# Optimization experiments

Hardware: AMD Instinct MI355X
Metric: run time of the kernel (lower is better)

Reference implementation:

```python
import jax, jax.numpy as jnp
import numpy as np
import math

# dims: batch, in-channels, freq bins, frames(=cropsize), ffn dim, bands
B, C, BINS, W, FF, NB = 16, 8, 1024, 256, 2048, 4
EPS = 1e-5


def _ln(x, g, b):
    m = x.mean(-1, keepdims=True)
    v = ((x - m) ** 2).mean(-1, keepdims=True)
    return (x - m) / jnp.sqrt(v + EPS) * g + b


def _conv1d(x, w, groups=1):
    # x: [b, Cin, L], w: [Cout, Cin//groups, K], 'same' padding
    pad = (w.shape[-1] - 1) // 2
    return jax.lax.conv_general_dilated(
        x, w, (1,), [(pad, pad)],
        dimension_numbers=('NCH', 'OIH', 'NCH'), feature_group_count=groups)


def _mb_attn(x, mem, qw, qb, kw, kb, vw, vb, ow, ob, er, dist_w):
    # MultibandFrameAttention with skewed relative-position bias
    b, w, c = x.shape
    d = c // NB
    q = (x @ qw.T + qb).reshape(b, w, NB, d).transpose(0, 2, 1, 3)    # [b,nb,w,d]
    k = (mem @ kw.T + kb).reshape(b, w, NB, d).transpose(0, 2, 3, 1)  # [b,nb,d,w]
    v = (mem @ vw.T + vb).reshape(b, w, NB, d).transpose(0, 2, 1, 3)  # [b,nb,w,d]
    # skew trick: q @ er -> pad left on last dim -> transpose -> drop first row
    qer = jnp.einsum('bnwd,dc->bnwc', q, er)                           # [b,nb,w,W]
    skew = jnp.pad(qer, ((0, 0), (0, 0), (0, 0), (1, 0)))
    skew = skew.transpose(0, 1, 3, 2)[:, :, 1:, :]                     # [b,nb,W,w]
    idx = jnp.arange(w)
    dist = jnp.abs(idx[:, None] - idx[None, :]).astype(x.dtype) / 2.0  # [w,w]
    p = dist[None] * dist_w + skew                                     # [b,nb,w,w]
    qk = jnp.einsum('bnwd,bndk->bnwk', q, k) / math.sqrt(c)
    a = jax.nn.softmax(qk + p, axis=-1)
    o = jnp.einsum('bnwk,bnkd->bnwd', a, v).transpose(0, 2, 1, 3).reshape(b, w, c)
    return o @ ow.T + ob


def setup_inputs() -> dict:
    key = jax.random.key(0)
    ks = jax.random.split(key, 24)
    rn = lambda k, s, sc=0.02: jax.random.normal(k, s, dtype=jnp.float32) * sc
    d = BINS // NB
    ones = lambda n: jnp.ones((n,), jnp.float32)
    zeros = lambda n: jnp.zeros((n,), jnp.float32)
    return {
        'x': jax.random.normal(ks[0], (B, C, BINS, W), jnp.float32),
        'bott_w': rn(ks[1], (1, C), 0.3),
        'bn_g': ones(1), 'bn_b': zeros(1), 'bn_m': zeros(1), 'bn_v': ones(1),
        'glu_w': rn(ks[2], (2 * BINS, BINS)),
        'n1g': ones(BINS), 'n1b': zeros(BINS),
        'c1L_w': rn(ks[3], (2 * FF, BINS)),
        'c1R_w': rn(ks[4], (FF // 2, BINS, 3)),
        'n2g': ones(2 * FF), 'n2b': zeros(2 * FF),
        'c2dw_w': rn(ks[5], (2 * FF, 1, 9), 0.1),
        'c2pw_w': rn(ks[6], (FF // 2, 2 * FF)),
        'n3g': ones(BINS), 'n3b': zeros(BINS),
        'qw': rn(ks[7], (BINS, BINS)), 'qb': zeros(BINS),
        'kw': rn(ks[8], (BINS, BINS)), 'kb': zeros(BINS),
        'vw': rn(ks[9], (BINS, BINS)), 'vb': zeros(BINS),
        'ow': rn(ks[10], (BINS, BINS)), 'ob': zeros(BINS),
        'er': rn(ks[11], (d, W), 0.02),
        'dist_w': rn(ks[12], (NB, W, 1), 0.02),
        'n4g': ones(BINS), 'n4b': zeros(BINS),
        'c3_w': rn(ks[13], (2 * FF, BINS)),
        'c4_w': rn(ks[14], (BINS, 2 * FF)),
        'n5g': ones(BINS), 'n5b': zeros(BINS),
    }


def reference(x, bott_w, bn_g, bn_b, bn_m, bn_v, glu_w, n1g, n1b,
              c1L_w, c1R_w, n2g, n2b, c2dw_w, c2pw_w, n3g, n3b,
              qw, qb, kw, kb, vw, vb, ow, ob, er, dist_w,
              n4g, n4b, c3_w, c4_w, n5g, n5b):
    # bottleneck: Linear(C->1) over channel dim, BatchNorm2d(1) eval, ReLU
    h0 = jnp.einsum('bchw,oc->bohw', x, bott_w)                        # [b,1,bins,w]
    h0 = (h0 - bn_m[None, :, None, None]) / jnp.sqrt(bn_v[None, :, None, None] + EPS)
    h0 = jax.nn.relu(h0 * bn_g[None, :, None, None] + bn_b[None, :, None, None])
    xs = h0[:, 0].transpose(0, 2, 1)                                   # [b,w,bins]

    # GLU block
    g = xs @ glu_w.T
    a, bgate = g[..., :BINS], g[..., BINS:]
    xs = _ln(xs + a * jax.nn.sigmoid(bgate), n1g, n1b)

    # conv/linear FFN
    hL = jax.nn.relu(xs @ c1L_w.T)                                     # [b,w,2ff]
    hR = jax.nn.relu(_conv1d(xs.transpose(0, 2, 1), c1R_w).transpose(0, 2, 1))
    hR = jnp.pad(hR, ((0, 0), (0, 0), (0, hL.shape[2] - hR.shape[2])))
    h = _ln(hL + hR, n2g, n2b)
    t = _conv1d(h.transpose(0, 2, 1), c2dw_w, groups=2 * FF)           # depthwise
    t = jnp.einsum('bcl,oc->bol', t, c2pw_w).transpose(0, 2, 1)        # [b,w,ff//2]
    t = jnp.pad(t, ((0, 0), (0, 0), (0, xs.shape[2] - t.shape[2])))
    xs = _ln(xs + t, n3g, n3b)

    # multiband attention (self)
    h = _mb_attn(xs, xs, qw, qb, kw, kb, vw, vb, ow, ob, er, dist_w)
    xs = _ln(xs + h, n4g, n4b)

    # final FFN
    h = jax.nn.relu(xs @ c3_w.T) @ c4_w.T
    xs = _ln(xs + h, n5g, n5b)
    return xs.transpose(0, 2, 1)[:, None]                              # [b,1,bins,w]
```

## Files before the change

### kernel.cpp

```cpp
#include <hip/hip_runtime.h>
#include <hip/hip_bf16.h>

#define EPSF 1e-5f

typedef unsigned short u16;
typedef unsigned int   u32;
typedef __attribute__((ext_vector_type(8))) short bf16x8;
typedef __attribute__((ext_vector_type(4))) float f32x4;

__device__ __forceinline__ u16 f2bf(float f) {
    u32 u = __builtin_bit_cast(u32, f);
    u32 r = u + 0x7fffu + ((u >> 16) & 1u);
    return (u16)(r >> 16);
}
__device__ __forceinline__ float bf2f(u16 h) {
    return __builtin_bit_cast(float, (u32)h << 16);
}
__device__ __forceinline__ float4 bf4f(ushort4 v) {
    return make_float4(bf2f(v.x), bf2f(v.y), bf2f(v.z), bf2f(v.w));
}
__device__ __forceinline__ ushort4 f4bf(float a, float b, float c, float d) {
    ushort4 o; o.x = f2bf(a); o.y = f2bf(b); o.z = f2bf(c); o.w = f2bf(d); return o;
}
__device__ __forceinline__ void gld16(void* lds, const void* gsrc) {
    __builtin_amdgcn_global_load_lds(
        (const __attribute__((address_space(1))) u32*)gsrc,
        (__attribute__((address_space(3))) u32*)lds, 16, 0, 0);
}

__device__ __forceinline__ float wred_sum(float v) {
#pragma unroll
    for (int off = 32; off; off >>= 1) v += __shfl_xor(v, off, 64);
    return v;
}
__device__ __forceinline__ void block_red2(float& s1, float& s2, int tid) {
    __shared__ float red[8];
    s1 = wred_sum(s1); s2 = wred_sum(s2);
    const int lane = tid & 63, wid = tid >> 6;
    if (!lane) { red[wid] = s1; red[4 + wid] = s2; }
    __syncthreads();
    s1 = red[0] + red[1] + red[2] + red[3];
    s2 = red[4] + red[5] + red[6] + red[7];
}

struct SetupArgs {
    const float* ws[9]; u16* wd[9]; int wn[9];
    const float* c1r; u16* c1rd;
    const float* er;  u16* erd;
    const float* dw;  float* dwd;
    const float* qb;  const float* kb; const float* vb; float* bcat;
    u16* zp;
    int off[15];
};
__global__ __launch_bounds__(256)
void setup_k(SetupArgs a)
{
    const int b = blockIdx.x;
    int seg = 0;
    while (seg < 13 && b >= a.off[seg + 1]) ++seg;
    const int i = (b - a.off[seg]) * 256 + threadIdx.x;
    if (seg < 9) {
        if (i < a.wn[seg]) {
            const float4 v = ((const float4*)a.ws[seg])[i];
            ((ushort4*)a.wd[seg])[i] = f4bf(v.x, v.y, v.z, v.w);
        }
    } else if (seg == 9) {
        if (i < 3145728) {
            const int q = i / 3072, rem = i - q * 3072;
            const int ks = rem >> 10, ci = rem & 1023;
            a.c1rd[i] = f2bf(a.c1r[((long)q * 1024 + ci) * 3 + ks]);
        }
    } else if (seg == 10) {
        if (i < 65536) { const int c = i >> 8, d = i & 255; a.erd[i] = f2bf(a.er[d * 256 + c]); }
    } else if (seg == 11) {
        if (i < 36864) { const int k = i >> 12, c = i & 4095; a.dwd[i] = a.dw[c * 9 + k]; }
    } else if (seg == 12) {
        if (i < 3072) { const float* s = (i < 1024) ? a.qb : ((i < 2048) ? a.kb : a.vb); a.bcat[i] = s[i & 1023]; }
    } else {
        if (i < 8192) a.zp[i] = 0;
    }
}

__global__ __launch_bounds__(256)
void bottleneck_k(const float* __restrict__ x, const float* __restrict__ bw,
                  const float* __restrict__ bn_g, const float* __restrict__ bn_b,
                  const float* __restrict__ bn_m, const float* __restrict__ bn_v,
                  u16* __restrict__ xsb)
{
    __shared__ float tile[32][33];
    const int b = blockIdx.z, h0 = blockIdx.y * 32, w0 = blockIdx.x * 32;
    const int tid = threadIdx.x, c = tid & 31, r = tid >> 5;
    float wreg[8];
#pragma unroll
    for (int ch = 0; ch < 8; ++ch) wreg[ch] = bw[ch];
    const float sc = bn_g[0] * rsqrtf(bn_v[0] + EPSF);
    const float sh = bn_b[0] - bn_m[0] * sc;
#pragma unroll
    for (int it = 0; it < 4; ++it) {
        const int h = h0 + r + it * 8;
        const int w = w0 + c;
        float acc = 0.f;
#pragma unroll
        for (int ch = 0; ch < 8; ++ch)
            acc += x[(((long)b * 8 + ch) * 1024 + h) * 256 + w] * wreg[ch];
        tile[r + it * 8][c] = fmaxf(acc * sc + sh, 0.f);
    }
    __syncthreads();
#pragma unroll
    for (int it = 0; it < 4; ++it) {
        const int wl = r + it * 8;
        xsb[((long)b * 256 + w0 + wl) * 1024 + h0 + c] = f2bf(tile[c][wl]);
    }
}

template<int ACT, int OUTBF, int BIAS, int SPLITK>
__global__ __launch_bounds__(512, 2)
void gemm8_k(const u16* __restrict__ A, const u16* __restrict__ B,
             const float* __restrict__ bias, void* __restrict__ Cout,
             int N, int K , int lda, int ldb, long partStride)
{
    extern __shared__ u16 lds[];
    const int m0 = blockIdx.y * 256, n0 = blockIdx.x * 256;
    const int koff = (SPLITK > 1) ? blockIdx.z * K : 0;
    const int nt = K >> 6;
    const int tid = threadIdx.x;
    const int lane = tid & 63, wid = tid >> 6;
    const int wr = ((wid >> 2) & 1) * 128;
    const int wc = (wid & 3) * 64;
    const int l15 = lane & 15, l4 = lane >> 4;

    const u16* Ag = A + (long)m0 * lda + koff;
    const u16* Bg = B + (long)n0 * ldb + koff;

    auto stage = [&](const u16* g, int ld, int ldsbase, int kcol, int h) {
#pragma unroll
        for (int is = 0; is < 2; ++is) {
            const int r = h * 128 + is * 64 + (tid >> 3);
            const int sc = ((tid & 7) * 8) ^ (((r >> 2) & 1) << 4);
            gld16(&lds[ldsbase + h * 8192 + is * 4096 + tid * 8],
                  g + (long)r * ld + kcol + sc);
        }
    };
    auto frag = [&](int base, int row, int col) -> bf16x8 {
        return *(const bf16x8*)&lds[base + row * 64 + (col ^ (((row >> 2) & 1) << 4))];
    };

    f32x4 acc[8][4] = {};

    stage(Ag, lda, 0, 0, 0);
    stage(Ag, lda, 0, 0, 1);
    stage(Bg, ldb, 32768, 0, 0);
    stage(Bg, ldb, 32768, 0, 1);
    if (nt > 1) {
        stage(Bg, ldb, 49152, 64, 0);
        stage(Bg, ldb, 49152, 64, 1);
        stage(Ag, lda, 16384, 64, 0);
        asm volatile("s_waitcnt vmcnt(6)" ::: "memory");
    } else {
        asm volatile("s_waitcnt vmcnt(0)" ::: "memory");
    }
    __builtin_amdgcn_s_barrier();

    for (int kt = 0; kt < nt; ++kt) {
        const int cs = kt & 1;
        const int ab = cs * 16384;
        const int bb = 32768 + cs * 16384;
        const int abn = (cs ^ 1) * 16384;
        const int kc1 = (kt + 1) * 64, kc2 = (kt + 2) * 64;
        bf16x8 alo[4][2], ahi[4][2], b01[2][2], b23[2][2];

#pragma unroll
        for (int i = 0; i < 4; ++i)
#pragma unroll
            for (int kk = 0; kk < 2; ++kk)
                alo[i][kk] = frag(ab, wr + i * 16 + l15, kk * 32 + l4 * 8);
#pragma unroll
        for (int j = 0; j < 2; ++j)
#pragma unroll
            for (int kk = 0; kk < 2; ++kk)
                b01[j][kk] = frag(bb, wc + j * 16 + l15, kk * 32 + l4 * 8);
        if (kt + 1 < nt) stage(Ag, lda, abn, kc1, 1);
        __builtin_amdgcn_s_barrier();
        asm volatile("s_waitcnt lgkmcnt(0)" ::: "memory");
        __builtin_amdgcn_s_setprio(1);
#pragma unroll
        for (int i = 0; i < 4; ++i)
#pragma unroll
            for (int j = 0; j < 2; ++j)
#pragma unroll
                for (int kk = 0; kk < 2; ++kk)
                    acc[i][j] = __builtin_amdgcn_mfma_f32_16x16x32_bf16(alo[i][kk], b01[j][kk], acc[i][j], 0, 0, 0);
        __builtin_amdgcn_s_setprio(0);
        __builtin_amdgcn_s_barrier();

#pragma unroll
        for (int j = 0; j < 2; ++j)
#pragma unroll
            for (int kk = 0; kk < 2; ++kk)
                b23[j][kk] = frag(bb, wc + (j + 2) * 16 + l15, kk * 32 + l4 * 8);
        if (kt + 2 < nt) stage(Bg, ldb, bb, kc2, 0);
        __builtin_amdgcn_s_barrier();
        asm volatile("s_waitcnt lgkmcnt(0)" ::: "memory");
        __builtin_amdgcn_s_setprio(1);
#pragma unroll
        for (int i = 0; i < 4; ++i)
#pragma unroll
            for (int j = 0; j < 2; ++j)
#pragma unroll
                for (int kk = 0; kk < 2; ++kk)
                    acc[i][j + 2] = __builtin_amdgcn_mfma_f32_16x16x32_bf16(alo[i][kk], b23[j][kk], acc[i][j + 2], 0, 0, 0);
        __builtin_amdgcn_s_setprio(0);
        __builtin_amdgcn_s_barrier();

#pragma unroll
        for (int i = 0; i < 4; ++i)
#pragma unroll
            for (int kk = 0; kk < 2; ++kk)
                ahi[i][kk] = frag(ab, wr + (i + 4) * 16 + l15, kk * 32 + l4 * 8);
        if (kt + 2 < nt) stage(Bg, ldb, bb, kc2, 1);
        __builtin_amdgcn_s_barrier();
        asm volatile("s_waitcnt lgkmcnt(0)" ::: "memory");
        __builtin_amdgcn_s_setprio(1);
#pragma unroll
        for (int i = 0; i < 4; ++i)
#pragma unroll
            for (int j = 0; j < 2; ++j)
#pragma unroll
                for (int kk = 0; kk < 2; ++kk)
                    acc[i + 4][j + 2] = __builtin_amdgcn_mfma_f32_16x16x32_bf16(ahi[i][kk], b23[j][kk], acc[i + 4][j + 2], 0, 0, 0);
        __builtin_amdgcn_s_setprio(0);
        __builtin_amdgcn_s_barrier();

        if (kt + 2 < nt) stage(Ag, lda, ab, kc2, 0);
        __builtin_amdgcn_s_barrier();
        __builtin_amdgcn_s_setprio(1);
#pragma unroll
        for (int i = 0; i < 4; ++i)
#pragma unroll
            for (int j = 0; j < 2; ++j)
#pragma unroll
                for (int kk = 0; kk < 2; ++kk)
                    acc[i + 4][j] = __builtin_amdgcn_mfma_f32_16x16x32_bf16(ahi[i][kk], b01[j][kk], acc[i + 4][j], 0, 0, 0);
        __builtin_amdgcn_s_setprio(0);
        if (kt + 2 < nt) {
            asm volatile("s_waitcnt vmcnt(6)" ::: "memory");
        } else {
            asm volatile("s_waitcnt vmcnt(0)" ::: "memory");
        }
        __builtin_amdgcn_s_barrier();
    }

    if (SPLITK > 1) {
        u16* Cp = (u16*)Cout + (long)blockIdx.z * partStride;
#pragma unroll
        for (int i = 0; i < 8; ++i)
#pragma unroll
            for (int j = 0; j < 4; ++j) {
                const int n = n0 + wc + j * 16 + l15;
#pragma unroll
                for (int q = 0; q < 4; ++q) {
                    const int m = m0 + wr + i * 16 + l4 * 4 + q;
                    Cp[(long)m * N + n] = f2bf(acc[i][j][q]);
                }
            }
    } else {
        float* Cf = (float*)Cout;
        u16*   Cb = (u16*)Cout;
#pragma unroll
        for (int i = 0; i < 8; ++i)
#pragma unroll
            for (int j = 0; j < 4; ++j) {
                const int n = n0 + wc + j * 16 + l15;
                const float bv = BIAS ? bias[n] : 0.f;
#pragma unroll
                for (int q = 0; q < 4; ++q) {
                    const int m = m0 + wr + i * 16 + l4 * 4 + q;
                    float v = acc[i][j][q] + bv;
                    if (ACT) v = fmaxf(v, 0.f);
                    if (OUTBF) Cb[(long)m * N + n] = f2bf(v);
                    else       Cf[(long)m * N + n] = v;
                }
            }
    }
}

__global__ __launch_bounds__(512, 2)
void conv38_k(const u16* __restrict__ Xb, const u16* __restrict__ Wt,
              const u16* __restrict__ zp, u16* __restrict__ C)
{
    extern __shared__ u16 lds[];
    const int ks = blockIdx.z;
    const int m0 = blockIdx.y * 256, n0 = blockIdx.x * 256;
    const int nt = 16;
    const int tid = threadIdx.x;
    const int lane = tid & 63, wid = tid >> 6;
    const int wr = ((wid >> 2) & 1) * 128;
    const int wc = (wid & 3) * 64;
    const int l15 = lane & 15, l4 = lane >> 4;

    auto stageA = [&](int ldsbase, int kcol, int h) {
#pragma unroll
        for (int is = 0; is < 2; ++is) {
            const int r = h * 128 + is * 64 + (tid >> 3);
            const int sc = ((tid & 7) * 8) ^ (((r >> 2) & 1) << 4);
            const int t = m0 + r;
            const int wp = (t & 255) + ks - 1;
            const u16* src = ((unsigned)wp < 256u)
                ? Xb + (long)(t + ks - 1) * 1024 + kcol + sc
                : zp;
            gld16(&lds[ldsbase + h * 8192 + is * 4096 + tid * 8], src);
        }
    };
    auto stageB = [&](int ldsbase, int kcol, int h) {
#pragma unroll
        for (int is = 0; is < 2; ++is) {
            const int r = h * 128 + is * 64 + (tid >> 3);
            const int sc = ((tid & 7) * 8) ^ (((r >> 2) & 1) << 4);
            gld16(&lds[ldsbase + h * 8192 + is * 4096 + tid * 8],
                  Wt + (long)(n0 + r) * 3072 + ks * 1024 + kcol + sc);
        }
    };
    auto frag = [&](int base, int row, int col) -> bf16x8 {
        return *(const bf16x8*)&lds[base + row * 64 + (col ^ (((row >> 2) & 1) << 4))];
    };

    f32x4 acc[8][4] = {};

    stageA(0, 0, 0);
    stageA(0, 0, 1);
    stageB(32768, 0, 0);
    stageB(32768, 0, 1);
    stageB(49152, 64, 0);
    stageB(49152, 64, 1);
    stageA(16384, 64, 0);
    asm volatile("s_waitcnt vmcnt(6)" ::: "memory");
    __builtin_amdgcn_s_barrier();

    for (int kt = 0; kt < nt; ++kt) {
        const int cs = kt & 1;
        const int ab = cs * 16384;
        const int bb = 32768 + cs * 16384;
        const int abn = (cs ^ 1) * 16384;
        const int kc1 = (kt + 1) * 64, kc2 = (kt + 2) * 64;
        bf16x8 alo[4][2], ahi[4][2], b01[2][2], b23[2][2];

#pragma unroll
        for (int i = 0; i < 4; ++i)
#pragma unroll
            for (int kk = 0; kk < 2; ++kk)
                alo[i][kk] = frag(ab, wr + i * 16 + l15, kk * 32 + l4 * 8);
#pragma unroll
        for (int j = 0; j < 2; ++j)
#pragma unroll
            for (int kk = 0; kk < 2; ++kk)
                b01[j][kk] = frag(bb, wc + j * 16 + l15, kk * 32 + l4 * 8);
        if (kt + 1 < nt) stageA(abn, kc1, 1);
        __builtin_amdgcn_s_barrier();
        asm volatile("s_waitcnt lgkmcnt(0)" ::: "memory");
        __builtin_amdgcn_s_setprio(1);
#pragma unroll
        for (int i = 0; i < 4; ++i)
#pragma unroll
            for (int j = 0; j < 2; ++j)
#pragma unroll
                for (int kk = 0; kk < 2; ++kk)
                    acc[i][j] = __builtin_amdgcn_mfma_f32_16x16x32_bf16(alo[i][kk], b01[j][kk], acc[i][j], 0, 0, 0);
        __builtin_amdgcn_s_setprio(0);
        __builtin_amdgcn_s_barrier();

#pragma unroll
        for (int j = 0; j < 2; ++j)
#pragma unroll
            for (int kk = 0; kk < 2; ++kk)
                b23[j][kk] = frag(bb, wc + (j + 2) * 16 + l15, kk * 32 + l4 * 8);
        if (kt + 2 < nt) stageB(bb, kc2, 0);
        __builtin_amdgcn_s_barrier();
        asm volatile("s_waitcnt lgkmcnt(0)" ::: "memory");
        __builtin_amdgcn_s_setprio(1);
#pragma unroll
        for (int i = 0; i < 4; ++i)
#pragma unroll
            for (int j = 0; j < 2; ++j)
#pragma unroll
                for (int kk = 0; kk < 2; ++kk)
                    acc[i][j + 2] = __builtin_amdgcn_mfma_f32_16x16x32_bf16(alo[i][kk], b23[j][kk], acc[i][j + 2], 0, 0, 0);
        __builtin_amdgcn_s_setprio(0);
        __builtin_amdgcn_s_barrier();

#pragma unroll
        for (int i = 0; i < 4; ++i)
#pragma unroll
            for (int kk = 0; kk < 2; ++kk)
                ahi[i][kk] = frag(ab, wr + (i + 4) * 16 + l15, kk * 32 + l4 * 8);
        if (kt + 2 < nt) stageB(bb, kc2, 1);
        __builtin_amdgcn_s_barrier();
        asm volatile("s_waitcnt lgkmcnt(0)" ::: "memory");
        __builtin_amdgcn_s_setprio(1);
#pragma unroll
        for (int i = 0; i < 4; ++i)
#pragma unroll
            for (int j = 0; j < 2; ++j)
#pragma unroll
                for (int kk = 0; kk < 2; ++kk)
                    acc[i + 4][j + 2] = __builtin_amdgcn_mfma_f32_16x16x32_bf16(ahi[i][kk], b23[j][kk], acc[i + 4][j + 2], 0, 0, 0);
        __builtin_amdgcn_s_setprio(0);
        __builtin_amdgcn_s_barrier();

        if (kt + 2 < nt) stageA(ab, kc2, 0);
        __builtin_amdgcn_s_barrier();
        __builtin_amdgcn_s_setprio(1);
#pragma unroll
        for (int i = 0; i < 4; ++i)
#pragma unroll
            for (int j = 0; j < 2; ++j)
#pragma unroll
                for (int kk = 0; kk < 2; ++kk)
                    acc[i + 4][j] = __builtin_amdgcn_mfma_f32_16x16x32_bf16(ahi[i][kk], b01[j][kk], acc[i + 4][j], 0, 0, 0);
        __builtin_amdgcn_s_setprio(0);
        if (kt + 2 < nt) {
            asm volatile("s_waitcnt vmcnt(6)" ::: "memory");
        } else {
            asm volatile("s_waitcnt vmcnt(0)" ::: "memory");
        }
        __builtin_amdgcn_s_barrier();
    }

    u16* Cp = C + (long)ks * 4194304;
#pragma unroll
    for (int i = 0; i < 8; ++i)
#pragma unroll
        for (int j = 0; j < 4; ++j) {
            const int n = n0 + wc + j * 16 + l15;
#pragma unroll
            for (int q = 0; q < 4; ++q) {
                const int m = m0 + wr + i * 16 + l4 * 4 + q;
                Cp[(long)m * 1024 + n] = f2bf(acc[i][j][q]);
            }
        }
}

__global__ __launch_bounds__(256, 2)
void attn_fused_k(const u16* __restrict__ QKVb, const u16* __restrict__ erT,
                  const u16* __restrict__ Vt, const float* __restrict__ dwp,
                  u16* __restrict__ Oc)
{
    __shared__ __align__(16) u16 As[4096];
    __shared__ __align__(16) u16 Bs[16384];
    __shared__ __align__(16) u16 Pl[16384];
    __shared__ float redM[4][64];
    __shared__ float redS[4][64];
    const int z = blockIdx.y, zb = z >> 2, zn = z & 3;
    const int m0 = blockIdx.x * 64;
    const int tid = threadIdx.x;
    const int lane = tid & 63, wid = tid >> 6;
    const int l15 = lane & 15, l4 = lane >> 4;

    const u16* Qg = QKVb + (long)(zb * 256) * 3072 + zn * 256;
    const u16* Kg = Qg + 1024;

    auto stageA64 = [&](const u16* g, long ld) {
#pragma unroll
        for (int p = 0; p < 2; ++p) {
            const int e = p * 2048 + tid * 8;
            const int r = e >> 6, c = e & 63;
            const int sc = c ^ (((r >> 2) & 1) << 4);
            gld16(&As[e], g + (long)r * ld + sc);
        }
    };
    auto stageB256 = [&](const u16* g, long ld) {
#pragma unroll
        for (int p = 0; p < 8; ++p) {
            const int e = p * 2048 + tid * 8;
            const int r = e >> 6, c = e & 63;
            const int sc = c ^ (((r >> 2) & 1) << 4);
            gld16(&Bs[e], g + (long)r * ld + sc);
        }
    };
    auto fragA = [&](int i, int kk) -> bf16x8 {
        const int row = i * 16 + l15, col = kk * 32 + l4 * 8;
        return *(const bf16x8*)&As[row * 64 + (col ^ (((row >> 2) & 1) << 4))];
    };
    auto fragB = [&](int j, int kk) -> bf16x8 {
        const int row = wid * 64 + j * 16 + l15, col = kk * 32 + l4 * 8;
        return *(const bf16x8*)&Bs[row * 64 + (col ^ (((row >> 2) & 1) << 4))];
    };
    auto fragP = [&](int kc, int i, int kk) -> bf16x8 {
        const int row = i * 16 + l15, col = kk * 32 + l4 * 8;
        return *(const bf16x8*)&Pl[kc * 4096 + row * 64 + (col ^ (((row >> 2) & 1) << 4))];
    };

    f32x4 acc1[4][4] = {};
    f32x4 acc2[4][4] = {};

    for (int kc = 0; kc < 4; ++kc) {
        __syncthreads();
        stageA64(Qg + (long)m0 * 3072 + kc * 64, 3072);
        stageB256(Kg + kc * 64, 3072);
        __syncthreads();
#pragma unroll
        for (int i = 0; i < 4; ++i) {
            const bf16x8 a0 = fragA(i, 0), a1 = fragA(i, 1);
#pragma unroll
            for (int j = 0; j < 4; ++j) {
                acc1[i][j] = __builtin_amdgcn_mfma_f32_16x16x32_bf16(a0, fragB(j, 0), acc1[i][j], 0, 0, 0);
                acc1[i][j] = __builtin_amdgcn_mfma_f32_16x16x32_bf16(a1, fragB(j, 1), acc1[i][j], 0, 0, 0);
            }
        }
    }
    for (int kc = 0; kc < 4; ++kc) {
        __syncthreads();
        stageA64(erT + (long)m0 * 256 + kc * 64, 256);
        stageB256(Qg + kc * 64, 3072);
        __syncthreads();
#pragma unroll
        for (int i = 0; i < 4; ++i) {
            const bf16x8 a0 = fragA(i, 0), a1 = fragA(i, 1);
#pragma unroll
            for (int j = 0; j < 4; ++j) {
                acc2[i][j] = __builtin_amdgcn_mfma_f32_16x16x32_bf16(a0, fragB(j, 0), acc2[i][j], 0, 0, 0);
                acc2[i][j] = __builtin_amdgcn_mfma_f32_16x16x32_bf16(a1, fragB(j, 1), acc2[i][j], 0, 0, 0);
            }
        }
    }

    const float inv32 = 1.f / 32.f;
#pragma unroll
    for (int i = 0; i < 4; ++i)
#pragma unroll
        for (int q = 0; q < 4; ++q) {
            const int mg = m0 + i * 16 + l4 * 4 + q;
            const float dw = dwp[zn * 256 + mg];
#pragma unroll
            for (int j = 0; j < 4; ++j) {
                const int ng = wid * 64 + j * 16 + l15;
                acc1[i][j][q] = acc1[i][j][q] * inv32 + acc2[i][j][q]
                              + fabsf((float)(mg - ng)) * 0.5f * dw;
            }
        }

    float rmax[4][4], rsum[4][4];
#pragma unroll
    for (int i = 0; i < 4; ++i)
#pragma unroll
        for (int q = 0; q < 4; ++q) {
            float mv = fmaxf(fmaxf(acc1[i][0][q], acc1[i][1][q]),
                             fmaxf(acc1[i][2][q], acc1[i][3][q]));
#pragma unroll
            for (int off = 1; off <= 8; off <<= 1) mv = fmaxf(mv, __shfl_xor(mv, off, 64));
            rmax[i][q] = mv;
        }
    if (l15 == 0) {
#pragma unroll
        for (int i = 0; i < 4; ++i)
#pragma unroll
            for (int q = 0; q < 4; ++q)
                redM[wid][i * 16 + l4 * 4 + q] = rmax[i][q];
    }
    __syncthreads();
#pragma unroll
    for (int i = 0; i < 4; ++i)
#pragma unroll
        for (int q = 0; q < 4; ++q) {
            const int ml = i * 16 + l4 * 4 + q;
            rmax[i][q] = fmaxf(fmaxf(redM[0][ml], redM[1][ml]), fmaxf(redM[2][ml], redM[3][ml]));
        }
#pragma unroll
    for (int i = 0; i < 4; ++i)
#pragma unroll
        for (int q = 0; q < 4; ++q) {
            float sv = 0.f;
#pragma unroll
            for (int j = 0; j < 4; ++j) {
                const float e = __expf(acc1[i][j][q] - rmax[i][q]);
                acc1[i][j][q] = e;
                sv += e;
            }
#pragma unroll
            for (int off = 1; off <= 8; off <<= 1) sv += __shfl_xor(sv, off, 64);
            rsum[i][q] = sv;
        }
    if (l15 == 0) {
#pragma unroll
        for (int i = 0; i < 4; ++i)
#pragma unroll
            for (int q = 0; q < 4; ++q)
                redS[wid][i * 16 + l4 * 4 + q] = rsum[i][q];
    }
    __syncthreads();
#pragma unroll
    for (int i = 0; i < 4; ++i)
#pragma unroll
        for (int q = 0; q < 4; ++q) {
            const int ml = i * 16 + l4 * 4 + q;
            rsum[i][q] = redS[0][ml] + redS[1][ml] + redS[2][ml] + redS[3][ml];
        }
#pragma unroll
    for (int i = 0; i < 4; ++i)
#pragma unroll
        for (int q = 0; q < 4; ++q) {
            const float rinv = 1.f / rsum[i][q];
            const int ml = i * 16 + l4 * 4 + q;
#pragma unroll
            for (int j = 0; j < 4; ++j) {
                const int nc = j * 16 + l15;
                Pl[wid * 4096 + ml * 64 + (nc ^ (((ml >> 2) & 1) << 4))] = f2bf(acc1[i][j][q] * rinv);
            }
        }
    __syncthreads();

    f32x4 accO[4][4] = {};
    for (int kc = 0; kc < 4; ++kc) {
        __syncthreads();
        stageB256(Vt + (long)(z * 256) * 256 + kc * 64, 256);
        __syncthreads();
#pragma unroll
        for (int i = 0; i < 4; ++i) {
            const bf16x8 a0 = fragP(kc, i, 0), a1 = fragP(kc, i, 1);
#pragma unroll
            for (int j = 0; j < 4; ++j) {
                accO[i][j] = __builtin_amdgcn_mfma_f32_16x16x32_bf16(a0, fragB(j, 0), accO[i][j], 0, 0, 0);
                accO[i][j] = __builtin_amdgcn_mfma_f32_16x16x32_bf16(a1, fragB(j, 1), accO[i][j], 0, 0, 0);
            }
        }
    }

#pragma unroll
    for (int i = 0; i < 4; ++i)
#pragma unroll
        for (int j = 0; j < 4; ++j) {
            const int d = wid * 64 + j * 16 + l15;
#pragma unroll
            for (int q = 0; q < 4; ++q) {
                const int mg = m0 + i * 16 + l4 * 4 + q;
                Oc[(long)(zb * 256 + mg) * 1024 + zn * 256 + d] = f2bf(accO[i][j][q]);
            }
        }
}

__global__ __launch_bounds__(256)
void glu_ln_k(const u16* __restrict__ xs0, const u16* __restrict__ g2,
              const float* __restrict__ gam, const float* __restrict__ bet,
              u16* __restrict__ outb)
{
    const int t = blockIdx.x, tid = threadIdx.x;
    const int f0 = tid * 4;
    const long PS = 8388608;
    const float4 xv = bf4f(*(const ushort4*)&xs0[(long)t * 1024 + f0]);
    const float4 a0 = bf4f(*(const ushort4*)&g2[(long)t * 2048 + f0]);
    const float4 g0 = bf4f(*(const ushort4*)&g2[(long)t * 2048 + 1024 + f0]);
    const float4 a1 = bf4f(*(const ushort4*)&g2[PS + (long)t * 2048 + f0]);
    const float4 g1 = bf4f(*(const ushort4*)&g2[PS + (long)t * 2048 + 1024 + f0]);
    const float ax = a0.x + a1.x, ay = a0.y + a1.y, az = a0.z + a1.z, aw = a0.w + a1.w;
    const float gx = g0.x + g1.x, gy = g0.y + g1.y, gz = g0.z + g1.z, gw = g0.w + g1.w;
    float vals[4];
    vals[0] = xv.x + ax / (1.f + expf(-gx));
    vals[1] = xv.y + ay / (1.f + expf(-gy));
    vals[2] = xv.z + az / (1.f + expf(-gz));
    vals[3] = xv.w + aw / (1.f + expf(-gw));
    float s1 = vals[0] + vals[1] + vals[2] + vals[3];
    float s2 = vals[0]*vals[0] + vals[1]*vals[1] + vals[2]*vals[2] + vals[3]*vals[3];
    block_red2(s1, s2, tid);
    const float mean = s1 * (1.f / 1024.f);
    const float var  = s2 * (1.f / 1024.f) - mean * mean;
    const float rstd = rsqrtf(var + EPSF);
    const float4 gm = *(const float4*)&gam[f0];
    const float4 bt = *(const float4*)&bet[f0];
    *(ushort4*)&outb[(long)t * 1024 + f0] = f4bf(
        (vals[0] - mean) * rstd * gm.x + bt.x,
        (vals[1] - mean) * rstd * gm.y + bt.y,
        (vals[2] - mean) * rstd * gm.z + bt.z,
        (vals[3] - mean) * rstd * gm.w + bt.w);
}

template<int P, int BIAS>
__global__ __launch_bounds__(256)
void add_ln1024_k(const u16* __restrict__ A, const u16* __restrict__ Bp,
                  const float* __restrict__ bias,
                  const float* __restrict__ gam, const float* __restrict__ bet,
                  u16* __restrict__ outb)
{
    const int t = blockIdx.x, tid = threadIdx.x;
    const int f0 = tid * 4;
    const long PS = 4194304;
    const float4 a = bf4f(*(const ushort4*)&A[(long)t * 1024 + f0]);
    float4 b = bf4f(*(const ushort4*)&Bp[(long)t * 1024 + f0]);
#pragma unroll
    for (int p = 1; p < P; ++p) {
        const float4 bp = bf4f(*(const ushort4*)&Bp[p * PS + (long)t * 1024 + f0]);
        b.x += bp.x; b.y += bp.y; b.z += bp.z; b.w += bp.w;
    }
    if (BIAS) {
        const float4 bb = *(const float4*)&bias[f0];
        b.x += bb.x; b.y += bb.y; b.z += bb.z; b.w += bb.w;
    }
    float vals[4] = {a.x + b.x, a.y + b.y, a.z + b.z, a.w + b.w};
    float s1 = vals[0] + vals[1] + vals[2] + vals[3];
    float s2 = vals[0]*vals[0] + vals[1]*vals[1] + vals[2]*vals[2] + vals[3]*vals[3];
    block_red2(s1, s2, tid);
    const float mean = s1 * (1.f / 1024.f);
    const float var  = s2 * (1.f / 1024.f) - mean * mean;
    const float rstd = rsqrtf(var + EPSF);
    const float4 gm = *(const float4*)&gam[f0];
    const float4 bt = *(const float4*)&bet[f0];
    *(ushort4*)&outb[(long)t * 1024 + f0] = f4bf(
        (vals[0] - mean) * rstd * gm.x + bt.x,
        (vals[1] - mean) * rstd * gm.y + bt.y,
        (vals[2] - mean) * rstd * gm.z + bt.z,
        (vals[3] - mean) * rstd * gm.w + bt.w);
}

__global__ __launch_bounds__(256)
void add_ln4096_k(const u16* __restrict__ A, const u16* __restrict__ Bp,
                  const float* __restrict__ gam, const float* __restrict__ bet,
                  u16* __restrict__ outb)
{
    const int t = blockIdx.x, tid = threadIdx.x;
    const long PS = 4194304;
    const int f0 = tid * 16;
    float vals[16];
    const bf16x8 a0 = *(const bf16x8*)&A[(long)t * 4096 + f0];
    const bf16x8 a1 = *(const bf16x8*)&A[(long)t * 4096 + f0 + 8];
#pragma unroll
    for (int e = 0; e < 8; ++e) { vals[e] = bf2f((u16)a0[e]); vals[8 + e] = bf2f((u16)a1[e]); }
    if (tid < 64) {
#pragma unroll
        for (int c = 0; c < 4; ++c) {
            const int fc = f0 + c * 4;
            const float4 b0 = bf4f(*(const ushort4*)&Bp[(long)t * 1024 + fc]);
            const float4 b1 = bf4f(*(const ushort4*)&Bp[PS + (long)t * 1024 + fc]);
            const float4 b2 = bf4f(*(const ushort4*)&Bp[2 * PS + (long)t * 1024 + fc]);
            vals[c*4+0] += fmaxf(b0.x + b1.x + b2.x, 0.f);
            vals[c*4+1] += fmaxf(b0.y + b1.y + b2.y, 0.f);
            vals[c*4+2] += fmaxf(b0.z + b1.z + b2.z, 0.f);
            vals[c*4+3] += fmaxf(b0.w + b1.w + b2.w, 0.f);
        }
    }
    float s1 = 0.f, s2 = 0.f;
#pragma unroll
    for (int e = 0; e < 16; ++e) { s1 += vals[e]; s2 += vals[e] * vals[e]; }
    block_red2(s1, s2, tid);
    const float mean = s1 * (1.f / 4096.f);
    const float var  = s2 * (1.f / 4096.f) - mean * mean;
    const float rstd = rsqrtf(var + EPSF);
#pragma unroll
    for (int c = 0; c < 4; ++c) {
        const int fc = f0 + c * 4;
        const float4 gm = *(const float4*)&gam[fc];
        const float4 bt = *(const float4*)&bet[fc];
        *(ushort4*)&outb[(long)t * 4096 + fc] = f4bf(
            (vals[c*4+0] - mean) * rstd * gm.x + bt.x,
            (vals[c*4+1] - mean) * rstd * gm.y + bt.y,
            (vals[c*4+2] - mean) * rstd * gm.z + bt.z,
            (vals[c*4+3] - mean) * rstd * gm.w + bt.w);
    }
}

__global__ __launch_bounds__(256)
void dwconv8_k(const u16* __restrict__ h, const float* __restrict__ wT,
               u16* __restrict__ out)
{
    const long idx = (long)blockIdx.x * 256 + threadIdx.x;
    const int cg = (int)(idx & 511);
    const int t  = (int)(idx >> 9);
    const int w  = t & 255;
    const int c0 = cg * 8;
    float acc[8] = {};
#pragma unroll
    for (int k = 0; k < 9; ++k) {
        const int wp = w + k - 4;
        if ((unsigned)wp < 256u) {
            const bf16x8 hv = *(const bf16x8*)&h[(long)(t + k - 4) * 4096 + c0];
            const float4 w0 = *(const float4*)&wT[k * 4096 + c0];
            const float4 w1 = *(const float4*)&wT[k * 4096 + c0 + 4];
            acc[0] += bf2f((u16)hv[0]) * w0.x;
            acc[1] += bf2f((u16)hv[1]) * w0.y;
            acc[2] += bf2f((u16)hv[2]) * w0.z;
            acc[3] += bf2f((u16)hv[3]) * w0.w;
            acc[4] += bf2f((u16)hv[4]) * w1.x;
            acc[5] += bf2f((u16)hv[5]) * w1.y;
            acc[6] += bf2f((u16)hv[6]) * w1.z;
            acc[7] += bf2f((u16)hv[7]) * w1.w;
        }
    }
    bf16x8 res;
#pragma unroll
    for (int j = 0; j < 8; ++j) res[j] = (short)f2bf(acc[j]);
    *(bf16x8*)&out[(long)t * 4096 + c0] = res;
}

__global__ __launch_bounds__(256)
void vtrans_k(const u16* __restrict__ QKVb, u16* __restrict__ Vt)
{
    __shared__ u16 t[32][33];
    const int z = blockIdx.z, zb = z >> 2, zn = z & 3;
    const int w0 = blockIdx.x * 32, d0 = blockIdx.y * 32;
    const int tid = threadIdx.x, c = tid & 31, r = tid >> 5;
#pragma unroll
    for (int it = 0; it < 4; ++it) {
        const int wl = r + it * 8;
        t[wl][c] = QKVb[(long)(zb * 256 + w0 + wl) * 3072 + 2048 + zn * 256 + d0 + c];
    }
    __syncthreads();
#pragma unroll
    for (int it = 0; it < 4; ++it) {
        const int dl = r + it * 8;
        Vt[((long)z * 256 + d0 + dl) * 256 + w0 + c] = t[c][dl];
    }
}

__global__ __launch_bounds__(256)
void transpose_out_k(const u16* __restrict__ xs, float* __restrict__ out)
{
    __shared__ u16 tile[32][34];
    const int b = blockIdx.z, f0 = blockIdx.y * 32, w0 = blockIdx.x * 32;
    const int tid = threadIdx.x, c = tid & 31, r = tid >> 5;
#pragma unroll
    for (int it = 0; it < 4; ++it) {
        const int w = w0 + r + it * 8;
        tile[r + it * 8][c] = xs[((long)b * 256 + w) * 1024 + f0 + c];
    }
    __syncthreads();
#pragma unroll
    for (int it = 0; it < 4; ++it) {
        const int fl = r + it * 8;
        out[((long)b * 1024 + f0 + fl) * 256 + w0 + c] = bf2f(tile[c][fl]);
    }
}

extern "C" void kernel_launch(void* const* d_in, const int* in_sizes, int n_in,
                              void* d_out, int out_size, void* d_ws, size_t ws_size,
                              hipStream_t stream)
{
    const float* x      = (const float*)d_in[0];
    const float* bott_w = (const float*)d_in[1];
    const float* bn_g   = (const float*)d_in[2];
    const float* bn_b   = (const float*)d_in[3];
    const float* bn_m   = (const float*)d_in[4];
    const float* bn_v   = (const float*)d_in[5];
    const float* glu_w  = (const float*)d_in[6];
    const float* n1g    = (const float*)d_in[7];
    const float* n1b    = (const float*)d_in[8];
    const float* c1L_w  = (const float*)d_in[9];
    const float* c1R_w  = (const float*)d_in[10];
    const float* n2g    = (const float*)d_in[11];
    const float* n2b    = (const float*)d_in[12];
    const float* c2dw_w = (const float*)d_in[13];
    const float* c2pw_w = (const float*)d_in[14];
    const float* n3g    = (const float*)d_in[15];
    const float* n3b    = (const float*)d_in[16];
    const float* qw     = (const float*)d_in[17];
    const float* qb     = (const float*)d_in[18];
    const float* kw     = (const float*)d_in[19];
    const float* kb     = (const float*)d_in[20];
    const float* vw     = (const float*)d_in[21];
    const float* vb     = (const float*)d_in[22];
    const float* ow     = (const float*)d_in[23];
    const float* ob     = (const float*)d_in[24];
    const float* er     = (const float*)d_in[25];
    const float* dist_w = (const float*)d_in[26];
    const float* n4g    = (const float*)d_in[27];
    const float* n4b    = (const float*)d_in[28];
    const float* c3_w   = (const float*)d_in[29];
    const float* c4_w   = (const float*)d_in[30];
    const float* n5g    = (const float*)d_in[31];
    const float* n5b    = (const float*)d_in[32];
    float* out = (float*)d_out;

    char* Wb_ = (char*)d_ws;
    auto Bf = [&](size_t mib) { return (u16*)(Wb_ + (mib << 20)); };
    u16* XA   = Bf(0);
    u16* XB   = Bf(8);
    u16* H0b  = Bf(32);
    u16* Hglu = Bf(64);
    u16* C3p  = Bf(64);
    u16* P4   = Bf(64);
    u16* H1b  = Bf(128);
    u16* Hdw  = Bf(160);
    u16* QKVb = Bf(192);
    u16* Vt   = Bf(216);
    u16* S1b  = Bf(264);
    u16* wGLU = Bf(296); u16* wC1L = Bf(300); u16* wC1R = Bf(308);
    u16* wC2P = Bf(314); u16* wQKV = Bf(322); u16* wO   = Bf(328);
    u16* wC3  = Bf(330); u16* wC4  = Bf(338);
    u16* erT  = Bf(346);
    u16* zp   = (u16*)(Wb_ + (346u << 20) + 131072);
    float* wdwT = (float*)(Wb_ + (346u << 20) + 131072 + 16384);
    float* bQKV = (float*)(Wb_ + (346u << 20) + 131072 + 16384 + 147456);

    const dim3 blk(256);
    const dim3 blk8(512);
    const long PS1 = 4194304;
    const size_t SH8 = 131072;

    SetupArgs sa;
    sa.ws[0] = glu_w;  sa.wd[0] = wGLU;            sa.wn[0] = 524288;
    sa.ws[1] = c1L_w;  sa.wd[1] = wC1L;            sa.wn[1] = 1048576;
    sa.ws[2] = c2pw_w; sa.wd[2] = wC2P;            sa.wn[2] = 1048576;
    sa.ws[3] = c3_w;   sa.wd[3] = wC3;             sa.wn[3] = 1048576;
    sa.ws[4] = c4_w;   sa.wd[4] = wC4;             sa.wn[4] = 1048576;
    sa.ws[5] = qw;     sa.wd[5] = wQKV;            sa.wn[5] = 262144;
    sa.ws[6] = kw;     sa.wd[6] = wQKV + 1048576;  sa.wn[6] = 262144;
    sa.ws[7] = vw;     sa.wd[7] = wQKV + 2097152;  sa.wn[7] = 262144;
    sa.ws[8] = ow;     sa.wd[8] = wO;              sa.wn[8] = 262144;
    sa.c1r = c1R_w; sa.c1rd = wC1R;
    sa.er  = er;    sa.erd  = erT;
    sa.dw  = c2dw_w; sa.dwd = wdwT;
    sa.qb = qb; sa.kb = kb; sa.vb = vb; sa.bcat = bQKV;
    sa.zp = zp;
    {
        int bc[14] = {2048, 4096, 4096, 4096, 4096, 1024, 1024, 1024, 1024,
                      12288, 256, 144, 12, 32};
        int acc = 0;
        for (int s = 0; s < 14; ++s) { sa.off[s] = acc; acc += bc[s]; }
        sa.off[14] = acc;
        setup_k<<<dim3(acc), blk, 0, stream>>>(sa);
    }

    bottleneck_k<<<dim3(8, 32, 16), blk, 0, stream>>>(x, bott_w, bn_g, bn_b, bn_m, bn_v, XA);

    gemm8_k<0,0,0,2><<<dim3(8, 16, 2), blk8, SH8, stream>>>(XA, wGLU, nullptr, Hglu,
        2048, 512, 1024, 1024, (long)4096 * 2048);

    glu_ln_k<<<dim3(4096), blk, 0, stream>>>(XA, Hglu, n1g, n1b, XB);

    gemm8_k<1,1,0,1><<<dim3(16, 16, 1), blk8, SH8, stream>>>(XB, wC1L, nullptr, H0b,
        4096, 1024, 1024, 1024, 0);

    conv38_k<<<dim3(4, 16, 3), blk8, SH8, stream>>>(XB, wC1R, zp, C3p);

    add_ln4096_k<<<dim3(4096), blk, 0, stream>>>(H0b, C3p, n2g, n2b, H1b);

    dwconv8_k<<<dim3(8192), blk, 0, stream>>>(H1b, wdwT, Hdw);

    gemm8_k<0,0,0,4><<<dim3(4, 16, 4), blk8, SH8, stream>>>(Hdw, wC2P, nullptr, P4,
        1024, 1024, 4096, 4096, PS1);

    add_ln1024_k<4,0><<<dim3(4096), blk, 0, stream>>>(XB, P4, nullptr, n3g, n3b, XA);

    gemm8_k<0,1,1,1><<<dim3(12, 16, 1), blk8, SH8, stream>>>(XA, wQKV, bQKV, QKVb,
        3072, 1024, 1024, 1024, 0);

    vtrans_k<<<dim3(8, 8, 64), blk, 0, stream>>>(QKVb, Vt);

    attn_fused_k<<<dim3(4, 64), blk, 0, stream>>>(QKVb, erT, Vt, dist_w, S1b);

    gemm8_k<0,0,0,4><<<dim3(4, 16, 4), blk8, SH8, stream>>>(S1b, wO, nullptr, P4,
        1024, 256, 1024, 1024, PS1);

    add_ln1024_k<4,1><<<dim3(4096), blk, 0, stream>>>(XA, P4, ob, n4g, n4b, XB);

    gemm8_k<1,1,0,1><<<dim3(16, 16, 1), blk8, SH8, stream>>>(XB, wC3, nullptr, H0b,
        4096, 1024, 1024, 1024, 0);

    gemm8_k<0,0,0,4><<<dim3(4, 16, 4), blk8, SH8, stream>>>(H0b, wC4, nullptr, P4,
        1024, 1024, 4096, 4096, PS1);

    add_ln1024_k<4,0><<<dim3(4096), blk, 0, stream>>>(XB, P4, nullptr, n5g, n5b, XA);

    transpose_out_k<<<dim3(8, 32, 16), blk, 0, stream>>>(XA, out);

    (void)in_sizes; (void)n_in; (void)out_size; (void)ws_size;
}
```

Before: 496.4 us.

## Merge FFN linear GEMM with conv GEMM launch; fold QK scale into K weights

Combines the c1L ReLU GEMM and the three-tap conv GEMM into one kernel launch with a 28x16 grid. Blocks with index below 16 compute the linear branch and the rest compute one conv tap, which removes a launch and lets both workloads share one wave of blocks. Separately, the 1/32 attention scale is folded into the K projection weights and bias at setup. This lets the attention kernel accumulate QK and Q·er into a single accumulator array, freeing registers. The trade-off is that the scaled K is rounded to bf16 after scaling, and each block carries some divergent setup logic.

```diff
diff --git a/kernel.cpp b/kernel.cpp
--- a/kernel.cpp
+++ b/kernel.cpp
@@ -62,7 +62,8 @@
     if (seg < 9) {
         if (i < a.wn[seg]) {
             const float4 v = ((const float4*)a.ws[seg])[i];
-            ((ushort4*)a.wd[seg])[i] = f4bf(v.x, v.y, v.z, v.w);
+            const float s = (seg == 6) ? 0.03125f : 1.f;
+            ((ushort4*)a.wd[seg])[i] = f4bf(v.x * s, v.y * s, v.z * s, v.w * s);
         }
     } else if (seg == 9) {
         if (i < 3145728) {
@@ -75,7 +76,12 @@
     } else if (seg == 11) {
         if (i < 36864) { const int k = i >> 12, c = i & 4095; a.dwd[i] = a.dw[c * 9 + k]; }
     } else if (seg == 12) {
-        if (i < 3072) { const float* s = (i < 1024) ? a.qb : ((i < 2048) ? a.kb : a.vb); a.bcat[i] = s[i & 1023]; }
+        if (i < 3072) {
+            const float* s = (i < 1024) ? a.qb : ((i < 2048) ? a.kb : a.vb);
+            float v = s[i & 1023];
+            if (i >= 1024 && i < 2048) v *= 0.03125f;
+            a.bcat[i] = v;
+        }
     } else {
         if (i < 8192) a.zp[i] = 0;
     }
@@ -285,12 +291,20 @@
 }
 
 __global__ __launch_bounds__(512, 2)
-void conv38_k(const u16* __restrict__ Xb, const u16* __restrict__ Wt,
-              const u16* __restrict__ zp, u16* __restrict__ C)
+void ffconv8_k(const u16* __restrict__ Xb, const u16* __restrict__ Wl,
+               const u16* __restrict__ Wr, const u16* __restrict__ zp,
+               u16* __restrict__ Hout, u16* __restrict__ Cp3)
 {
     extern __shared__ u16 lds[];
-    const int ks = blockIdx.z;
-    const int m0 = blockIdx.y * 256, n0 = blockIdx.x * 256;
+    const int bx = blockIdx.x;
+    const int m0 = blockIdx.y * 256;
+    const bool conv = bx >= 16;
+    const int tap  = conv ? ((bx - 16) >> 2) : 0;
+    const int shift = conv ? (tap - 1) : 0;
+    const int n0 = conv ? (((bx - 16) & 3) * 256) : (bx * 256);
+    const u16* Bbase = conv ? (Wr + (long)n0 * 3072 + tap * 1024)
+                            : (Wl + (long)n0 * 1024);
+    const int ldb = conv ? 3072 : 1024;
     const int nt = 16;
     const int tid = threadIdx.x;
     const int lane = tid & 63, wid = tid >> 6;
@@ -304,9 +318,9 @@
             const int r = h * 128 + is * 64 + (tid >> 3);
             const int sc = ((tid & 7) * 8) ^ (((r >> 2) & 1) << 4);
             const int t = m0 + r;
-            const int wp = (t & 255) + ks - 1;
+            const int wp = (t & 255) + shift;
             const u16* src = ((unsigned)wp < 256u)
-                ? Xb + (long)(t + ks - 1) * 1024 + kcol + sc
+                ? Xb + (long)(t + shift) * 1024 + kcol + sc
                 : zp;
             gld16(&lds[ldsbase + h * 8192 + is * 4096 + tid * 8], src);
         }
@@ -317,7 +331,7 @@
             const int r = h * 128 + is * 64 + (tid >> 3);
             const int sc = ((tid & 7) * 8) ^ (((r >> 2) & 1) << 4);
             gld16(&lds[ldsbase + h * 8192 + is * 4096 + tid * 8],
-                  Wt + (long)(n0 + r) * 3072 + ks * 1024 + kcol + sc);
+                  Bbase + (long)r * ldb + kcol + sc);
         }
     };
     auto frag = [&](int base, int row, int col) -> bf16x8 {
@@ -425,18 +439,32 @@
         __builtin_amdgcn_s_barrier();
     }
 
-    u16* Cp = C + (long)ks * 4194304;
-#pragma unroll
-    for (int i = 0; i < 8; ++i)
-#pragma unroll
-        for (int j = 0; j < 4; ++j) {
-            const int n = n0 + wc + j * 16 + l15;
-#pragma unroll
-            for (int q = 0; q < 4; ++q) {
-                const int m = m0 + wr + i * 16 + l4 * 4 + q;
-                Cp[(long)m * 1024 + n] = f2bf(acc[i][j][q]);
+    if (conv) {
+        u16* Cp = Cp3 + (long)tap * 4194304;
+#pragma unroll
+        for (int i = 0; i < 8; ++i)
+#pragma unroll
+            for (int j = 0; j < 4; ++j) {
+                const int n = n0 + wc + j * 16 + l15;
+#pragma unroll
+                for (int q = 0; q < 4; ++q) {
+                    const int m = m0 + wr + i * 16 + l4 * 4 + q;
+                    Cp[(long)m * 1024 + n] = f2bf(acc[i][j][q]);
+                }
             }
-        }
+    } else {
+#pragma unroll
+        for (int i = 0; i < 8; ++i)
+#pragma unroll
+            for (int j = 0; j < 4; ++j) {
+                const int n = n0 + wc + j * 16 + l15;
+#pragma unroll
+                for (int q = 0; q < 4; ++q) {
+                    const int m = m0 + wr + i * 16 + l4 * 4 + q;
+                    Hout[(long)m * 4096 + n] = f2bf(fmaxf(acc[i][j][q], 0.f));
+                }
+            }
+    }
 }
 
 __global__ __launch_bounds__(256, 2)
@@ -490,12 +518,16 @@
     };
 
     f32x4 acc1[4][4] = {};
-    f32x4 acc2[4][4] = {};
-
-    for (int kc = 0; kc < 4; ++kc) {
+
+    for (int kc = 0; kc < 8; ++kc) {
         __syncthreads();
-        stageA64(Qg + (long)m0 * 3072 + kc * 64, 3072);
-        stageB256(Kg + kc * 64, 3072);
+        if (kc < 4) {
+            stageA64(Qg + (long)m0 * 3072 + kc * 64, 3072);
+            stageB256(Kg + kc * 64, 3072);
+        } else {
+            stageA64(erT + (long)m0 * 256 + (kc - 4) * 64, 256);
+            stageB256(Qg + (kc - 4) * 64, 3072);
+        }
         __syncthreads();
 #pragma unroll
         for (int i = 0; i < 4; ++i) {
@@ -507,23 +539,7 @@
             }
         }
     }
-    for (int kc = 0; kc < 4; ++kc) {
-        __syncthreads();
-        stageA64(erT + (long)m0 * 256 + kc * 64, 256);
-        stageB256(Qg + kc * 64, 3072);
-        __syncthreads();
-#pragma unroll
-        for (int i = 0; i < 4; ++i) {
-            const bf16x8 a0 = fragA(i, 0), a1 = fragA(i, 1);
-#pragma unroll
-            for (int j = 0; j < 4; ++j) {
-                acc2[i][j] = __builtin_amdgcn_mfma_f32_16x16x32_bf16(a0, fragB(j, 0), acc2[i][j], 0, 0, 0);
-                acc2[i][j] = __builtin_amdgcn_mfma_f32_16x16x32_bf16(a1, fragB(j, 1), acc2[i][j], 0, 0, 0);
-            }
-        }
-    }
-
-    const float inv32 = 1.f / 32.f;
+
 #pragma unroll
     for (int i = 0; i < 4; ++i)
 #pragma unroll
@@ -533,8 +549,7 @@
 #pragma unroll
             for (int j = 0; j < 4; ++j) {
                 const int ng = wid * 64 + j * 16 + l15;
-                acc1[i][j][q] = acc1[i][j][q] * inv32 + acc2[i][j][q]
-                              + fabsf((float)(mg - ng)) * 0.5f * dw;
+                acc1[i][j][q] += fabsf((float)(mg - ng)) * 0.5f * dw;
             }
         }
 
@@ -923,10 +938,7 @@
 
     glu_ln_k<<<dim3(4096), blk, 0, stream>>>(XA, Hglu, n1g, n1b, XB);
 
-    gemm8_k<1,1,0,1><<<dim3(16, 16, 1), blk8, SH8, stream>>>(XB, wC1L, nullptr, H0b,
-        4096, 1024, 1024, 1024, 0);
-
-    conv38_k<<<dim3(4, 16, 3), blk8, SH8, stream>>>(XB, wC1R, zp, C3p);
+    ffconv8_k<<<dim3(28, 16), blk8, SH8, stream>>>(XB, wC1L, wC1R, zp, H0b, C3p);
 
     add_ln4096_k<<<dim3(4096), blk, 0, stream>>>(H0b, C3p, n2g, n2b, H1b);
 
```

After: 486.8 us. Within noise of the previous version (-1.9%).
